# Kernel tuning notes

Measured on AMD Instinct MI355X. Metric: run time of the kernel, lower is better.

## Reference

```python
import jax, jax.numpy as jnp
import numpy as np
import math

# adaptive_schedule(t=100): t_norm=0.9 -> n_clusters~417 -> 256 -> patch_size=2, k_neighbors=16 (static)
PATCH = 2
K_NEIGH = 16
WIN = 4  # int(sqrt(k_neighbors)) neighborhood window
HID = 1152
HEADS = 16
DH = HID // HEADS
IMG = 32
GRID = IMG // PATCH  # 16 -> 256 tokens
N = GRID * GRID
IN_CH = 4
OUT_CH = 8  # learn_sigma -> 2*in_channels
B = 16
L = 2
NUM_CLASSES = 1000


def _sincos_2d(dim, gs):
    def _1d(d, pos):
        omega = 1.0 / 10000 ** (np.arange(d // 2, dtype=np.float64) / (d / 2.0))
        out = np.einsum('m,d->md', pos.reshape(-1), omega)
        return np.concatenate([np.sin(out), np.cos(out)], axis=1)
    gh = np.arange(gs, dtype=np.float32)
    gw = np.arange(gs, dtype=np.float32)
    grid = np.stack(np.meshgrid(gw, gh), axis=0).reshape(2, -1)
    return np.concatenate([_1d(dim // 2, grid[0]), _1d(dim // 2, grid[1])], axis=1)


def setup_inputs():
    key = jax.random.key(0)
    ks = iter(jax.random.split(key, 32))
    s = 0.02
    d = {}
    d['x'] = jax.random.normal(next(ks), (B, IN_CH, IMG, IMG), jnp.float32)
    d['t'] = jnp.full((B,), 100.0, jnp.float32)  # fixed timestep -> adaptive_schedule -> (2, 16)
    d['y'] = jax.random.randint(next(ks), (B,), 0, NUM_CLASSES)
    d['pos_embed'] = jnp.asarray(_sincos_2d(HID, 4), jnp.float32)[None]  # (1,16,HID) original 4x4 grid
    d['patch_w'] = s * jax.random.normal(next(ks), (HID, IN_CH, PATCH, PATCH), jnp.float32)
    d['patch_b'] = jnp.zeros((HID,), jnp.float32)
    d['t_w1'] = s * jax.random.normal(next(ks), (256, HID), jnp.float32)
    d['t_b1'] = jnp.zeros((HID,), jnp.float32)
    d['t_w2'] = s * jax.random.normal(next(ks), (HID, HID), jnp.float32)
    d['t_b2'] = jnp.zeros((HID,), jnp.float32)
    d['y_table'] = s * jax.random.normal(next(ks), (NUM_CLASSES + 1, HID), jnp.float32)
    d['ada_w'] = s * jax.random.normal(next(ks), (L, HID, 6 * HID), jnp.float32)
    d['ada_b'] = jnp.zeros((L, 6 * HID), jnp.float32)
    d['qkv_w'] = s * jax.random.normal(next(ks), (L, HID, 3 * HID), jnp.float32)
    d['qkv_b'] = jnp.zeros((L, 3 * HID), jnp.float32)
    d['proj_w'] = s * jax.random.normal(next(ks), (L, HID, HID), jnp.float32)
    d['proj_b'] = jnp.zeros((L, HID), jnp.float32)
    d['mlp_w1'] = s * jax.random.normal(next(ks), (L, HID, 4 * HID), jnp.float32)
    d['mlp_b1'] = jnp.zeros((L, 4 * HID), jnp.float32)
    d['mlp_w2'] = s * jax.random.normal(next(ks), (L, 4 * HID, HID), jnp.float32)
    d['mlp_b2'] = jnp.zeros((L, HID), jnp.float32)
    d['fl_ada_w'] = s * jax.random.normal(next(ks), (HID, 2 * HID), jnp.float32)
    d['fl_ada_b'] = jnp.zeros((2 * HID,), jnp.float32)
    d['fl_w'] = s * jax.random.normal(next(ks), (HID, PATCH * PATCH * OUT_CH), jnp.float32)
    d['fl_b'] = jnp.zeros((PATCH * PATCH * OUT_CH,), jnp.float32)
    return d


def _ln(x, eps=1e-6):
    m = jnp.mean(x, -1, keepdims=True)
    v = jnp.var(x, -1, keepdims=True)
    return (x - m) * jax.lax.rsqrt(v + eps)


def _modulate(x, shift, scale):
    return x * (1 + scale[:, None]) + shift[:, None]


def _neighborhood_attn(x, qkv_w, qkv_b, proj_w, proj_b):
    # x: (B,N,C) laid out on GRIDxGRID; each query attends to a WINxWIN (=k_neighbors) window
    # clamped at borders (NATTEN-style shifted neighborhoods), avoiding any dense NxN score matrix.
    b = x.shape[0]
    qkv = (x @ qkv_w + qkv_b).reshape(b, GRID, GRID, 3, HEADS, DH)
    q, k, v = qkv[:, :, :, 0], qkv[:, :, :, 1], qkv[:, :, :, 2]  # (B,H,W,h,d)
    starts = jnp.clip(jnp.arange(GRID) - WIN // 2, 0, GRID - WIN)
    idx = starts[:, None] + jnp.arange(WIN)[None, :]

    def gather(a):
        a = a[:, idx]
        a = a[:, :, :, idx]
        return jnp.transpose(a, (0, 1, 3, 2, 4, 5, 6))

    kn, vn = gather(k), gather(v)
    scale = DH ** -0.5
    att = jnp.einsum('bijhd,bijpqhd->bijhpq', q * scale, kn).reshape(b, GRID, GRID, HEADS, WIN * WIN)
    att = jax.nn.softmax(att, axis=-1).reshape(b, GRID, GRID, HEADS, WIN, WIN)
    out = jnp.einsum('bijhpq,bijpqhd->bijhd', att, vn).reshape(b, N, HID)
    return out @ proj_w + proj_b


def reference(x, t, y, pos_embed, patch_w, patch_b, t_w1, t_b1, t_w2, t_b2, y_table,
              ada_w, ada_b, qkv_w, qkv_b, proj_w, proj_b, mlp_w1, mlp_b1, mlp_w2, mlp_b2,
              fl_ada_w, fl_ada_b, fl_w, fl_b):
    b = x.shape[0]
    # FlexiPatchEmbed at adaptive patch size (p=2)
    h = jax.lax.conv_general_dilated(x, patch_w, (PATCH, PATCH), 'VALID',
                                     dimension_numbers=('NCHW', 'OIHW', 'NCHW'))
    h = h.reshape(b, HID, N).transpose(0, 2, 1) + patch_b
    # resize_abs_pos_embed: 4x4 -> GRIDxGRID, bicubic
    pe = jax.image.resize(pos_embed.reshape(1, 4, 4, HID), (1, GRID, GRID, HID), method='bicubic')
    h = h + pe.reshape(1, N, HID)
    # TimestepEmbedder: sinusoidal (cos|sin) -> Linear, SiLU, Linear
    half = 128
    freqs = jnp.exp(-math.log(10000.0) * jnp.arange(half, dtype=jnp.float32) / half)
    args = t[:, None] * freqs[None]
    temb = jnp.concatenate([jnp.cos(args), jnp.sin(args)], axis=-1)
    temb = jax.nn.silu(temb @ t_w1 + t_b1) @ t_w2 + t_b2
    c = temb + y_table[y]  # eval mode: no label dropout
    for l in range(L):
        mod = jax.nn.silu(c) @ ada_w[l] + ada_b[l]
        sh1, sc1, g1, sh2, sc2, g2 = jnp.split(mod, 6, axis=-1)
        h = h + g1[:, None] * _neighborhood_attn(_modulate(_ln(h), sh1, sc1),
                                                 qkv_w[l], qkv_b[l], proj_w[l], proj_b[l])
        z = _modulate(_ln(h), sh2, sc2)
        z = jax.nn.gelu(z @ mlp_w1[l] + mlp_b1[l], approximate=True) @ mlp_w2[l] + mlp_b2[l]
        h = h + g2[:, None] * z
    # final_layer_ps_2 + unpatchify
    sh, sc = jnp.split(jax.nn.silu(c) @ fl_ada_w + fl_ada_b, 2, axis=-1)
    h = _modulate(_ln(h), sh, sc) @ fl_w + fl_b  # (B,N,p*p*OUT_CH)
    h = h.reshape(b, GRID, GRID, PATCH, PATCH, OUT_CH)
    return jnp.einsum('bhwpqc->bchpwq', h).reshape(b, OUT_CH, IMG, IMG)
```

## Files before the change

### kernel.cpp

```cpp
#include <hip/hip_runtime.h>
#include <cmath>

static constexpr int kHid = 1152;
static constexpr int kM   = 4096;

typedef __bf16 bf16x8 __attribute__((ext_vector_type(8)));
typedef float  f32x4  __attribute__((ext_vector_type(4)));

struct BicW { float w[16][4]; };

__device__ __forceinline__ float dev_silu(float x) { return x / (1.0f + expf(-x)); }
__device__ __forceinline__ float dev_gelu(float x) {
  float u = 0.7978845608028654f * (x + 0.044715f * x * x * x);
  return 0.5f * x * (1.0f + tanhf(u));
}

__device__ __forceinline__ void glds16(const void* g, void* l) {
  __builtin_amdgcn_global_load_lds(
      (const __attribute__((address_space(1))) unsigned int*)g,
      (__attribute__((address_space(3))) unsigned int*)l, 16, 0, 0);
}

__global__ __launch_bounds__(256) void k_patch_pos(
    const float* __restrict__ x, const float* __restrict__ pw,
    const float* __restrict__ pb, const float* __restrict__ pos,
    float* __restrict__ h, BicW W)
{
  const int total = kM * kHid;
  for (int idx = blockIdx.x * blockDim.x + threadIdx.x; idx < total;
       idx += gridDim.x * blockDim.x) {
    int c  = idx % kHid;
    int t  = idx / kHid;
    int b  = t >> 8;
    int gy = (t >> 4) & 15;
    int gx = t & 15;
    float acc = pb[c];
    const float* xb  = x + (size_t)b * 4 * 1024;
    const float* pwc = pw + (size_t)c * 16;
#pragma unroll
    for (int ic = 0; ic < 4; ic++)
#pragma unroll
      for (int p = 0; p < 2; p++)
#pragma unroll
        for (int q = 0; q < 2; q++)
          acc += xb[ic * 1024 + (gy * 2 + p) * 32 + gx * 2 + q] *
                 pwc[(ic * 2 + p) * 2 + q];
    float pe = 0.f;
#pragma unroll
    for (int iy = 0; iy < 4; iy++) {
      float ra = 0.f;
#pragma unroll
      for (int ix = 0; ix < 4; ix++)
        ra += W.w[gx][ix] * pos[(iy * 4 + ix) * kHid + c];
      pe += W.w[gy][iy] * ra;
    }
    h[idx] = acc + pe;
  }
}

__global__ __launch_bounds__(256) void k_temb1(
    const float* __restrict__ t, const float* __restrict__ w1,
    const float* __restrict__ b1, float* __restrict__ hid1)
{
  int b  = blockIdx.y;
  int j0 = blockIdx.x * 64;
  int tid = threadIdx.x;
  __shared__ float e[256];
  if (tid < 128) {
    float fr  = expf(-9.210340371976184f * (float)tid / 128.0f);
    float arg = t[b] * fr;
    e[tid]       = cosf(arg);
    e[tid + 128] = sinf(arg);
  }
  __syncthreads();
  int j = tid & 63, ks = tid >> 6;
  float acc = 0.f;
#pragma unroll 4
  for (int k = ks * 64; k < ks * 64 + 64; k++)
    acc += e[k] * w1[k * kHid + j0 + j];
  __shared__ float part[4][64];
  part[ks][j] = acc;
  __syncthreads();
  if (ks == 0) {
    float v = part[0][j] + part[1][j] + part[2][j] + part[3][j] + b1[j0 + j];
    hid1[b * kHid + j0 + j] = dev_silu(v);
  }
}

__global__ __launch_bounds__(256) void k_temb2(
    const float* __restrict__ hid1, const float* __restrict__ w2,
    const float* __restrict__ b2, const float* __restrict__ ytab,
    const int* __restrict__ y, float* __restrict__ c, float* __restrict__ sc)
{
  int b  = blockIdx.y;
  int j0 = blockIdx.x * 64;
  __shared__ float hs[kHid];
  for (int k = threadIdx.x; k < kHid; k += 256) hs[k] = hid1[b * kHid + k];
  __syncthreads();
  int j = threadIdx.x & 63, ks = threadIdx.x >> 6;
  float acc = 0.f;
#pragma unroll 4
  for (int k = ks * 288; k < ks * 288 + 288; k++)
    acc += hs[k] * w2[(size_t)k * kHid + j0 + j];
  __shared__ float part[4][64];
  part[ks][j] = acc;
  __syncthreads();
  if (ks == 0) {
    int jj = j0 + j;
    float v = part[0][j] + part[1][j] + part[2][j] + part[3][j] + b2[jj] +
              ytab[(size_t)y[b] * kHid + jj];
    c[b * kHid + jj]  = v;
    sc[b * kHid + jj] = dev_silu(v);
  }
}

__global__ __launch_bounds__(256) void k_ada(
    const float* __restrict__ scb, const float* __restrict__ w,
    const float* __restrict__ bias, float* __restrict__ out, int Nout)
{
  int b  = blockIdx.y;
  int j0 = blockIdx.x * 64;
  __shared__ float cs[kHid];
  for (int k = threadIdx.x; k < kHid; k += 256) cs[k] = scb[b * kHid + k];
  __syncthreads();
  int j = threadIdx.x & 63, ks = threadIdx.x >> 6;
  float acc = 0.f;
#pragma unroll 4
  for (int k = ks * 288; k < ks * 288 + 288; k++)
    acc += cs[k] * w[(size_t)k * Nout + j0 + j];
  __shared__ float part[4][64];
  part[ks][j] = acc;
  __syncthreads();
  if (ks == 0)
    out[(size_t)b * Nout + j0 + j] =
        part[0][j] + part[1][j] + part[2][j] + part[3][j] + bias[j0 + j];
}

__global__ __launch_bounds__(256) void k_convw(
    const float* __restrict__ W, __bf16* __restrict__ Wt, int K, int N)
{
  __shared__ float tile[32][33];
  int n0 = blockIdx.x * 32;
  int k0 = blockIdx.y * 32;
  int c = threadIdx.x & 31, r = threadIdx.x >> 5;
#pragma unroll
  for (int i = 0; i < 32; i += 8)
    tile[r + i][c] = W[(size_t)(k0 + r + i) * N + n0 + c];
  __syncthreads();
#pragma unroll
  for (int i = 0; i < 32; i += 8) {
    int nn = r + i;
    Wt[(size_t)(n0 + nn) * K + k0 + c] = (__bf16)tile[c][nn];
  }
}

__global__ __launch_bounds__(256) void k_ln_mod(
    const float* __restrict__ h, const float* __restrict__ mod, int mstride,
    int sh_off, int sc_off, __bf16* __restrict__ out)
{
  int token = blockIdx.x;
  int b = token >> 8;
  const float* x = h + (size_t)token * kHid;
  float s = 0.f, ss = 0.f;
  for (int c = threadIdx.x; c < kHid; c += 256) {
    float v = x[c]; s += v; ss += v * v;
  }
#pragma unroll
  for (int o = 32; o > 0; o >>= 1) {
    s += __shfl_down(s, o, 64); ss += __shfl_down(ss, o, 64);
  }
  __shared__ float red[2][4];
  __shared__ float stats[2];
  int wave = threadIdx.x >> 6, lane = threadIdx.x & 63;
  if (lane == 0) { red[0][wave] = s; red[1][wave] = ss; }
  __syncthreads();
  if (threadIdx.x == 0) {
    float S  = red[0][0] + red[0][1] + red[0][2] + red[0][3];
    float SS = red[1][0] + red[1][1] + red[1][2] + red[1][3];
    float mean = S * (1.0f / kHid);
    float var  = SS * (1.0f / kHid) - mean * mean;
    stats[0] = mean;
    stats[1] = rsqrtf(var + 1e-6f);
  }
  __syncthreads();
  float mean = stats[0], rstd = stats[1];
  const float* shv = mod + (size_t)b * mstride + sh_off;
  const float* scv = mod + (size_t)b * mstride + sc_off;
  __bf16* o = out + (size_t)token * kHid;
  for (int c = threadIdx.x; c < kHid; c += 256) {
    float v = (x[c] - mean) * rstd;
    o[c] = (__bf16)(v * (1.f + scv[c]) + shv[c]);
  }
}

template<int RB, int CB, int MODE, typename OutT>
__global__ __launch_bounds__(256) void mfma_gemm(
    const __bf16* __restrict__ A, const __bf16* __restrict__ Wt,
    const float* __restrict__ bias, OutT* __restrict__ C,
    const float* __restrict__ gate, int gstride, int K, int Nout)
{
  constexpr int BM = RB * 32;
  constexpr int BN = CB * 32;
  __shared__ __attribute__((aligned(16))) __bf16 As[BM * 32];
  __shared__ __attribute__((aligned(16))) __bf16 Bs[BN * 32];

  const int tid  = threadIdx.x;
  const int lane = tid & 63;
  const int wv   = tid >> 6;
  const int wy   = wv >> 1, wx = wv & 1;
  const int l15  = lane & 15;
  const int quad = lane >> 4;
  const int m0   = blockIdx.y * BM;
  const int n0   = blockIdx.x * BN;

  f32x4 acc[RB][CB] = {};

  const int arow0 = tid >> 2;
  const int akc   = (tid & 3) * 8;

  for (int k0 = 0; k0 < K; k0 += 32) {
#pragma unroll
    for (int p = 0; p < BM / 64; p++) {
      int row = arow0 + p * 64;
      glds16(A + (size_t)(m0 + row) * K + k0 + akc, &As[(row * 32) + akc]);
    }
#pragma unroll
    for (int p = 0; p < BN / 64; p++) {
      int row = arow0 + p * 64;
      glds16(Wt + (size_t)(n0 + row) * K + k0 + akc, &Bs[(row * 32) + akc]);
    }
    __syncthreads();

    bf16x8 af[RB], bf[CB];
#pragma unroll
    for (int r = 0; r < RB; r++)
      af[r] = *(const bf16x8*)&As[(wy * RB * 16 + r * 16 + l15) * 32 + quad * 8];
#pragma unroll
    for (int c2 = 0; c2 < CB; c2++)
      bf[c2] = *(const bf16x8*)&Bs[(wx * CB * 16 + c2 * 16 + l15) * 32 + quad * 8];
#pragma unroll
    for (int r = 0; r < RB; r++)
#pragma unroll
      for (int c2 = 0; c2 < CB; c2++)
        acc[r][c2] = __builtin_amdgcn_mfma_f32_16x16x32_bf16(af[r], bf[c2], acc[r][c2], 0, 0, 0);
    __syncthreads();
  }

  const int bidx = m0 >> 8;
#pragma unroll
  for (int c2 = 0; c2 < CB; c2++) {
    int col = n0 + wx * CB * 16 + c2 * 16 + l15;
    float bcol = bias[col];
    float gv = (MODE == 2) ? gate[(size_t)bidx * gstride + col] : 0.f;
#pragma unroll
    for (int r = 0; r < RB; r++) {
      int mbase = m0 + wy * RB * 16 + r * 16 + quad * 4;
#pragma unroll
      for (int reg = 0; reg < 4; reg++) {
        float v = acc[r][c2][reg] + bcol;
        size_t off = (size_t)(mbase + reg) * Nout + col;
        if (MODE == 0) C[off] = (OutT)v;
        if (MODE == 1) C[off] = (OutT)dev_gelu(v);
        if (MODE == 2) C[off] = C[off] + (OutT)(gv * v);
      }
    }
  }
}

__global__ __launch_bounds__(256) void k_attn(const __bf16* __restrict__ qkv,
                                              __bf16* __restrict__ out)
{
  int token = blockIdx.x;
  int b = token >> 8;
  int i = (token >> 4) & 15;
  int j = token & 15;
  int si = min(max(i - 2, 0), 12);
  int sj = min(max(j - 2, 0), 12);
  __shared__ float att[16][17];
  __shared__ float prob[16][17];

  int hh = threadIdx.x >> 4;
  int pq = threadIdx.x & 15;
  int ni = si + (pq >> 2);
  int nj = sj + (pq & 3);
  int ntok = (b << 8) | (ni << 4) | nj;
  const __bf16* qp = qkv + (size_t)token * 3456 + hh * 72;
  const __bf16* kp = qkv + (size_t)ntok  * 3456 + kHid + hh * 72;
  float s = 0.f;
#pragma unroll
  for (int dc = 0; dc < 9; dc++) {
    bf16x8 qv = *(const bf16x8*)(qp + dc * 8);
    bf16x8 kv = *(const bf16x8*)(kp + dc * 8);
#pragma unroll
    for (int d = 0; d < 8; d++) s += (float)qv[d] * (float)kv[d];
  }
  att[hh][pq] = s * 0.11785113019775793f;
  __syncthreads();
  if (threadIdx.x < 16) {
    int hd = threadIdx.x;
    float m = att[hd][0];
    for (int e2 = 1; e2 < 16; e2++) m = fmaxf(m, att[hd][e2]);
    float sum = 0.f;
    for (int e2 = 0; e2 < 16; e2++) {
      float ex = expf(att[hd][e2] - m);
      prob[hd][e2] = ex;
      sum += ex;
    }
    float inv = 1.f / sum;
    for (int e2 = 0; e2 < 16; e2++) prob[hd][e2] *= inv;
  }
  __syncthreads();
  if (threadIdx.x < 144) {
    int hd = threadIdx.x / 9;
    int dc = threadIdx.x - hd * 9;
    float a8[8] = {};
#pragma unroll
    for (int e2 = 0; e2 < 16; e2++) {
      int nt = (b << 8) | ((si + (e2 >> 2)) << 4) | (sj + (e2 & 3));
      bf16x8 vv = *(const bf16x8*)(qkv + (size_t)nt * 3456 + 2304 + hd * 72 + dc * 8);
      float p = prob[hd][e2];
#pragma unroll
      for (int d = 0; d < 8; d++) a8[d] += p * (float)vv[d];
    }
    bf16x8 ov;
#pragma unroll
    for (int d = 0; d < 8; d++) ov[d] = (__bf16)a8[d];
    *(bf16x8*)(out + (size_t)token * kHid + hd * 72 + dc * 8) = ov;
  }
}

__global__ __launch_bounds__(256) void k_final(
    const float* __restrict__ h, const float* __restrict__ flm,
    const float* __restrict__ fw, const float* __restrict__ fb,
    float* __restrict__ out)
{
  int token = blockIdx.x;
  int b = token >> 8;
  const float* x = h + (size_t)token * kHid;
  float s = 0.f, ss = 0.f;
  for (int c = threadIdx.x; c < kHid; c += 256) { float v = x[c]; s += v; ss += v * v; }
#pragma unroll
  for (int o = 32; o > 0; o >>= 1) {
    s += __shfl_down(s, o, 64); ss += __shfl_down(ss, o, 64);
  }
  __shared__ float red[2][4];
  __shared__ float stats[2];
  __shared__ float xs[kHid];
  int wave = threadIdx.x >> 6, lane = threadIdx.x & 63;
  if (lane == 0) { red[0][wave] = s; red[1][wave] = ss; }
  __syncthreads();
  if (threadIdx.x == 0) {
    float S  = red[0][0] + red[0][1] + red[0][2] + red[0][3];
    float SS = red[1][0] + red[1][1] + red[1][2] + red[1][3];
    float mean = S * (1.0f / kHid);
    float var  = SS * (1.0f / kHid) - mean * mean;
    stats[0] = mean; stats[1] = rsqrtf(var + 1e-6f);
  }
  __syncthreads();
  float mean = stats[0], rstd = stats[1];
  const float* shv = flm + (size_t)b * 2304;
  const float* scv = shv + kHid;
  for (int c = threadIdx.x; c < kHid; c += 256)
    xs[c] = ((x[c] - mean) * rstd) * (1.f + scv[c]) + shv[c];
  __syncthreads();
  if (threadIdx.x < 32) {
    int jj = threadIdx.x;
    float acc = fb[jj];
    for (int k = 0; k < kHid; k++) acc += xs[k] * fw[k * 32 + jj];
    int p = jj >> 4, q = (jj >> 3) & 1, cc = jj & 7;
    int gy = (token >> 4) & 15, gx = token & 15;
    out[(((size_t)b * 8 + cc) * 32 + (gy * 2 + p)) * 32 + (gx * 2 + q)] = acc;
  }
}

extern "C" void kernel_launch(void* const* d_in, const int* in_sizes, int n_in,
                              void* d_out, int out_size, void* d_ws, size_t ws_size,
                              hipStream_t stream)
{
  const float* x        = (const float*)d_in[0];
  const float* t        = (const float*)d_in[1];
  const int*   y        = (const int*)  d_in[2];
  const float* pos      = (const float*)d_in[3];
  const float* patch_w  = (const float*)d_in[4];
  const float* patch_b  = (const float*)d_in[5];
  const float* t_w1     = (const float*)d_in[6];
  const float* t_b1     = (const float*)d_in[7];
  const float* t_w2     = (const float*)d_in[8];
  const float* t_b2     = (const float*)d_in[9];
  const float* y_table  = (const float*)d_in[10];
  const float* ada_w    = (const float*)d_in[11];
  const float* ada_b    = (const float*)d_in[12];
  const float* qkv_w    = (const float*)d_in[13];
  const float* qkv_b    = (const float*)d_in[14];
  const float* proj_w   = (const float*)d_in[15];
  const float* proj_b   = (const float*)d_in[16];
  const float* mlp_w1   = (const float*)d_in[17];
  const float* mlp_b1   = (const float*)d_in[18];
  const float* mlp_w2   = (const float*)d_in[19];
  const float* mlp_b2   = (const float*)d_in[20];
  const float* fl_ada_w = (const float*)d_in[21];
  const float* fl_ada_b = (const float*)d_in[22];
  const float* fl_w     = (const float*)d_in[23];
  const float* fl_b     = (const float*)d_in[24];
  float* out = (float*)d_out;

  float* ws   = (float*)d_ws;
  float*  h    = ws;
  __bf16* xmod = (__bf16*)(h + (size_t)4096 * 1152);
  __bf16* big  = xmod + (size_t)4096 * 1152;
  __bf16* wq   = big  + (size_t)4096 * 4608;
  __bf16* wp   = wq   + (size_t)3456 * 1152;
  __bf16* wm1  = wp   + (size_t)1152 * 1152;
  __bf16* wm2  = wm1  + (size_t)4608 * 1152;
  float*  cbuf = (float*)(wm2 + (size_t)1152 * 4608);
  float*  scb  = cbuf + 16 * 1152;
  float*  hid1 = scb  + 16 * 1152;
  float*  mod  = hid1 + 16 * 1152;
  float*  flm  = mod  + 16 * 6912;

  BicW W;
  for (int o = 0; o < 16; o++) {
    double sf = (o + 0.5) * 0.25 - 0.5;
    double wd[4]; double tot = 0.0;
    const double a = -0.5;
    for (int i = 0; i < 4; i++) {
      double d = fabs(sf - (double)i);
      double v;
      if (d <= 1.0)      v = ((a + 2.0) * d - (a + 3.0)) * d * d + 1.0;
      else if (d < 2.0)  v = a * (((d - 5.0) * d + 8.0) * d - 4.0);
      else               v = 0.0;
      wd[i] = v; tot += v;
    }
    for (int i = 0; i < 4; i++) W.w[o][i] = (float)(wd[i] / tot);
  }

  k_patch_pos<<<4608, 256, 0, stream>>>(x, patch_w, patch_b, pos, h, W);
  k_temb1<<<dim3(18, 16), 256, 0, stream>>>(t, t_w1, t_b1, hid1);
  k_temb2<<<dim3(18, 16), 256, 0, stream>>>(hid1, t_w2, t_b2, y_table, y, cbuf, scb);

  for (int l = 0; l < 2; l++) {
    k_convw<<<dim3(108, 36), 256, 0, stream>>>(qkv_w + (size_t)l * 1152 * 3456, wq, 1152, 3456);
    k_convw<<<dim3(36, 36),  256, 0, stream>>>(proj_w + (size_t)l * 1152 * 1152, wp, 1152, 1152);
    k_convw<<<dim3(144, 36), 256, 0, stream>>>(mlp_w1 + (size_t)l * 1152 * 4608, wm1, 1152, 4608);
    k_convw<<<dim3(36, 144), 256, 0, stream>>>(mlp_w2 + (size_t)l * 4608 * 1152, wm2, 4608, 1152);

    const float* ab = ada_b + (size_t)l * 6912;
    k_ada<<<dim3(108, 16), 256, 0, stream>>>(scb, ada_w + (size_t)l * 1152 * 6912, ab, mod, 6912);

    k_ln_mod<<<4096, 256, 0, stream>>>(h, mod, 6912, 0, 1152, xmod);
    mfma_gemm<4, 4, 0, __bf16><<<dim3(27, 32), 256, 0, stream>>>(
        xmod, wq, qkv_b + (size_t)l * 3456, big, nullptr, 0, 1152, 3456);
    k_attn<<<4096, 256, 0, stream>>>(big, xmod);
    mfma_gemm<4, 2, 2, float><<<dim3(18, 32), 256, 0, stream>>>(
        xmod, wp, proj_b + (size_t)l * 1152, h, mod + 2304, 6912, 1152, 1152);

    k_ln_mod<<<4096, 256, 0, stream>>>(h, mod, 6912, 3456, 4608, xmod);
    mfma_gemm<4, 4, 1, __bf16><<<dim3(36, 32), 256, 0, stream>>>(
        xmod, wm1, mlp_b1 + (size_t)l * 4608, big, nullptr, 0, 1152, 4608);
    mfma_gemm<4, 2, 2, float><<<dim3(18, 32), 256, 0, stream>>>(
        big, wm2, mlp_b2 + (size_t)l * 1152, h, mod + 5760, 6912, 4608, 1152);
  }

  k_ada<<<dim3(36, 16), 256, 0, stream>>>(scb, fl_ada_w, fl_ada_b, flm, 2304);
  k_final<<<4096, 256, 0, stream>>>(h, flm, fl_w, fl_b, out);
}
```

Before: 1.180 ms.

## Split-K residual GEMMs with atomic accumulation and merge weight-conversion launches

The proj and MLP-down GEMMs that accumulate into the fp32 residual now split K in two across blockIdx.z. Each slice adds its gated partial with an atomic add, and only slice 0 adds the bias. This doubles the block count for these 576-block launches so more of the CUs have work. The four per-layer weight transpose/convert launches are also merged into one kernel that picks its matrix from a descriptor table. Atomics make the float summation order nondeterministic and add contention on the write-back.

```diff
diff --git a/kernel.cpp b/kernel.cpp
--- a/kernel.cpp
+++ b/kernel.cpp
@@ -136,21 +136,29 @@
         part[0][j] + part[1][j] + part[2][j] + part[3][j] + bias[j0 + j];
 }
 
-__global__ __launch_bounds__(256) void k_convw(
-    const float* __restrict__ W, __bf16* __restrict__ Wt, int K, int N)
-{
+struct ConvDesc { const float* src; __bf16* dst; int K, N, tilesX; int start; };
+struct ConvDescs { ConvDesc d[4]; };
+
+__global__ __launch_bounds__(256) void k_convw4(ConvDescs cd)
+{
+  int bid = blockIdx.x;
+  int e = 0;
+#pragma unroll
+  for (int i = 1; i < 4; i++) if (bid >= cd.d[i].start) e = i;
+  const ConvDesc& D = cd.d[e];
+  int lid = bid - D.start;
+  int tx = lid % D.tilesX, ty = lid / D.tilesX;
+  int n0 = tx * 32, k0 = ty * 32;
   __shared__ float tile[32][33];
-  int n0 = blockIdx.x * 32;
-  int k0 = blockIdx.y * 32;
   int c = threadIdx.x & 31, r = threadIdx.x >> 5;
 #pragma unroll
   for (int i = 0; i < 32; i += 8)
-    tile[r + i][c] = W[(size_t)(k0 + r + i) * N + n0 + c];
+    tile[r + i][c] = D.src[(size_t)(k0 + r + i) * D.N + n0 + c];
   __syncthreads();
 #pragma unroll
   for (int i = 0; i < 32; i += 8) {
     int nn = r + i;
-    Wt[(size_t)(n0 + nn) * K + k0 + c] = (__bf16)tile[c][nn];
+    D.dst[(size_t)(n0 + nn) * D.K + k0 + c] = (__bf16)tile[c][nn];
   }
 }
 
@@ -196,8 +204,9 @@
 template<int RB, int CB, int MODE, typename OutT>
 __global__ __launch_bounds__(256) void mfma_gemm(
     const __bf16* __restrict__ A, const __bf16* __restrict__ Wt,
-    const float* __restrict__ bias, OutT* __restrict__ C,
-    const float* __restrict__ gate, int gstride, int K, int Nout)
+    const float* __restrict__ bias, OutT* C,
+    const float* __restrict__ gate, int gstride,
+    int Kslice, int Ktot, int Nout)
 {
   constexpr int BM = RB * 32;
   constexpr int BN = CB * 32;
@@ -212,22 +221,23 @@
   const int quad = lane >> 4;
   const int m0   = blockIdx.y * BM;
   const int n0   = blockIdx.x * BN;
+  const int kbase = blockIdx.z * Kslice;
 
   f32x4 acc[RB][CB] = {};
 
   const int arow0 = tid >> 2;
   const int akc   = (tid & 3) * 8;
 
-  for (int k0 = 0; k0 < K; k0 += 32) {
+  for (int k0 = kbase; k0 < kbase + Kslice; k0 += 32) {
 #pragma unroll
     for (int p = 0; p < BM / 64; p++) {
       int row = arow0 + p * 64;
-      glds16(A + (size_t)(m0 + row) * K + k0 + akc, &As[(row * 32) + akc]);
+      glds16(A + (size_t)(m0 + row) * Ktot + k0 + akc, &As[(row * 32) + akc]);
     }
 #pragma unroll
     for (int p = 0; p < BN / 64; p++) {
       int row = arow0 + p * 64;
-      glds16(Wt + (size_t)(n0 + row) * K + k0 + akc, &Bs[(row * 32) + akc]);
+      glds16(Wt + (size_t)(n0 + row) * Ktot + k0 + akc, &Bs[(row * 32) + akc]);
     }
     __syncthreads();
 
@@ -247,10 +257,11 @@
   }
 
   const int bidx = m0 >> 8;
+  const bool addb = (blockIdx.z == 0);
 #pragma unroll
   for (int c2 = 0; c2 < CB; c2++) {
     int col = n0 + wx * CB * 16 + c2 * 16 + l15;
-    float bcol = bias[col];
+    float bcol = addb ? bias[col] : 0.f;
     float gv = (MODE == 2) ? gate[(size_t)bidx * gstride + col] : 0.f;
 #pragma unroll
     for (int r = 0; r < RB; r++) {
@@ -261,7 +272,7 @@
         size_t off = (size_t)(mbase + reg) * Nout + col;
         if (MODE == 0) C[off] = (OutT)v;
         if (MODE == 1) C[off] = (OutT)dev_gelu(v);
-        if (MODE == 2) C[off] = C[off] + (OutT)(gv * v);
+        if (MODE == 2) unsafeAtomicAdd((float*)&C[off], gv * v);
       }
     }
   }
@@ -439,26 +450,28 @@
   k_temb2<<<dim3(18, 16), 256, 0, stream>>>(hid1, t_w2, t_b2, y_table, y, cbuf, scb);
 
   for (int l = 0; l < 2; l++) {
-    k_convw<<<dim3(108, 36), 256, 0, stream>>>(qkv_w + (size_t)l * 1152 * 3456, wq, 1152, 3456);
-    k_convw<<<dim3(36, 36),  256, 0, stream>>>(proj_w + (size_t)l * 1152 * 1152, wp, 1152, 1152);
-    k_convw<<<dim3(144, 36), 256, 0, stream>>>(mlp_w1 + (size_t)l * 1152 * 4608, wm1, 1152, 4608);
-    k_convw<<<dim3(36, 144), 256, 0, stream>>>(mlp_w2 + (size_t)l * 4608 * 1152, wm2, 4608, 1152);
+    ConvDescs cd;
+    cd.d[0] = { qkv_w  + (size_t)l * 1152 * 3456, wq,  1152, 3456, 108, 0 };
+    cd.d[1] = { proj_w + (size_t)l * 1152 * 1152, wp,  1152, 1152,  36, 3888 };
+    cd.d[2] = { mlp_w1 + (size_t)l * 1152 * 4608, wm1, 1152, 4608, 144, 3888 + 1296 };
+    cd.d[3] = { mlp_w2 + (size_t)l * 4608 * 1152, wm2, 4608, 1152,  36, 3888 + 1296 + 5184 };
+    k_convw4<<<3888 + 1296 + 5184 + 5184, 256, 0, stream>>>(cd);
 
     const float* ab = ada_b + (size_t)l * 6912;
     k_ada<<<dim3(108, 16), 256, 0, stream>>>(scb, ada_w + (size_t)l * 1152 * 6912, ab, mod, 6912);
 
     k_ln_mod<<<4096, 256, 0, stream>>>(h, mod, 6912, 0, 1152, xmod);
     mfma_gemm<4, 4, 0, __bf16><<<dim3(27, 32), 256, 0, stream>>>(
-        xmod, wq, qkv_b + (size_t)l * 3456, big, nullptr, 0, 1152, 3456);
+        xmod, wq, qkv_b + (size_t)l * 3456, big, nullptr, 0, 1152, 1152, 3456);
     k_attn<<<4096, 256, 0, stream>>>(big, xmod);
-    mfma_gemm<4, 2, 2, float><<<dim3(18, 32), 256, 0, stream>>>(
-        xmod, wp, proj_b + (size_t)l * 1152, h, mod + 2304, 6912, 1152, 1152);
+    mfma_gemm<4, 2, 2, float><<<dim3(18, 32, 2), 256, 0, stream>>>(
+        xmod, wp, proj_b + (size_t)l * 1152, h, mod + 2304, 6912, 576, 1152, 1152);
 
     k_ln_mod<<<4096, 256, 0, stream>>>(h, mod, 6912, 3456, 4608, xmod);
     mfma_gemm<4, 4, 1, __bf16><<<dim3(36, 32), 256, 0, stream>>>(
-        xmod, wm1, mlp_b1 + (size_t)l * 4608, big, nullptr, 0, 1152, 4608);
-    mfma_gemm<4, 2, 2, float><<<dim3(18, 32), 256, 0, stream>>>(
-        big, wm2, mlp_b2 + (size_t)l * 1152, h, mod + 5760, 6912, 4608, 1152);
+        xmod, wm1, mlp_b1 + (size_t)l * 4608, big, nullptr, 0, 1152, 1152, 4608);
+    mfma_gemm<4, 2, 2, float><<<dim3(18, 32, 2), 256, 0, stream>>>(
+        big, wm2, mlp_b2 + (size_t)l * 1152, h, mod + 5760, 6912, 2304, 4608, 1152);
   }
 
   k_ada<<<dim3(36, 16), 256, 0, stream>>>(scb, fl_ada_w, fl_ada_b, flm, 2304);
```

After: 1.240 ms. +5.1%, slower.
